# Performance work log

Hardware: AMD Instinct MI355X
Metric: run time of the kernel (lower is better)

The kernel has to match this reference:

```python
import jax, jax.numpy as jnp
import numpy as np

N = 16384      # total nodes (8 graphs x 2048)
E = 262144     # edges (avg degree 16)
TW = 25        # time_window
H = 128        # hidden_features
POS_DIM = 2
NB = 8         # number of graphs in batch
L = 6          # hidden_layer
DT = 0.01
EPS = 1e-5
MSG_IN = 2 * H + TW + POS_DIM + 1   # 284 (actual message concat width)
UPD_IN = H + H + 1                  # 257
EMB_IN = TW + POS_DIM + 1           # 28


def _lin(key, fan_in, fan_out):
    return jax.random.normal(key, (fan_in, fan_out), jnp.float32) / np.sqrt(fan_in)


def setup_inputs() -> dict:
    key = jax.random.key(0)
    ks = jax.random.split(key, 24)
    inp = {}
    inp["u"] = jax.random.normal(ks[0], (N, TW), jnp.float32)
    inp["pos"] = jax.random.uniform(ks[1], (N, 1 + POS_DIM), jnp.float32)
    inp["edge_index"] = jax.random.randint(ks[2], (2, E), 0, N)
    inp["batch"] = jnp.sort(jax.random.randint(ks[3], (N,), 0, NB))
    # embedding MLP
    inp["emb_W1"] = _lin(ks[4], EMB_IN, H); inp["emb_b1"] = jnp.zeros((H,), jnp.float32)
    inp["emb_W2"] = _lin(ks[5], H, H);      inp["emb_b2"] = jnp.zeros((H,), jnp.float32)
    # 6 GNN layers (stacked)
    inp["msg_W1"] = jax.vmap(lambda k: _lin(k, MSG_IN, H))(jax.random.split(ks[6], L))
    inp["msg_b1"] = jnp.zeros((L, H), jnp.float32)
    inp["msg_W2"] = jax.vmap(lambda k: _lin(k, H, H))(jax.random.split(ks[7], L))
    inp["msg_b2"] = jnp.zeros((L, H), jnp.float32)
    inp["upd_W1"] = jax.vmap(lambda k: _lin(k, UPD_IN, H))(jax.random.split(ks[8], L))
    inp["upd_b1"] = jnp.zeros((L, H), jnp.float32)
    inp["upd_W2"] = jax.vmap(lambda k: _lin(k, H, H))(jax.random.split(ks[9], L))
    inp["upd_b2"] = jnp.zeros((L, H), jnp.float32)
    # output CNN: Conv1d(1,8,15,s4) -> Conv1d(8,4,10,s2) -> Conv1d(4,1,10,s1)
    inp["conv1_W"] = jax.random.normal(ks[10], (8, 1, 15), jnp.float32) / np.sqrt(15)
    inp["conv1_b"] = jnp.zeros((8,), jnp.float32)
    inp["conv2_W"] = jax.random.normal(ks[11], (4, 8, 10), jnp.float32) / np.sqrt(80)
    inp["conv2_b"] = jnp.zeros((4,), jnp.float32)
    inp["conv3_W"] = jax.random.normal(ks[12], (1, 4, 10), jnp.float32) / np.sqrt(40)
    inp["conv3_b"] = jnp.zeros((1,), jnp.float32)
    return inp


def _mlp2(x, W1, b1, W2, b2):
    return jax.nn.relu(jax.nn.relu(x @ W1 + b1) @ W2 + b2)


def _instance_norm(h, batch):
    # PyG InstanceNorm (affine=False): per-graph, per-channel normalization
    cnt = jax.ops.segment_sum(jnp.ones((h.shape[0], 1), h.dtype), batch, NB)
    cnt = jnp.maximum(cnt, 1.0)
    mean = jax.ops.segment_sum(h, batch, NB) / cnt
    meansq = jax.ops.segment_sum(h * h, batch, NB) / cnt
    var = jnp.maximum(meansq - mean * mean, 0.0)
    return (h - mean[batch]) * jax.lax.rsqrt(var[batch] + EPS)


def _gnn_layer(h, u, pos_sp, variables, src, dst, batch,
               mW1, mb1, mW2, mb2, uW1, ub1, uW2, ub2):
    # message: gather endpoints, concat, 2-layer ReLU MLP  [E, MSG_IN] -> [E, H]
    m_in = jnp.concatenate([h[dst], h[src], u[dst] - u[src],
                            pos_sp[dst] - pos_sp[src], variables[dst]], axis=-1)
    msg = _mlp2(m_in, mW1, mb1, mW2, mb2)
    # mean-scatter aggregation onto target nodes
    deg = jax.ops.segment_sum(jnp.ones((src.shape[0], 1), h.dtype), dst, N)
    agg = jax.ops.segment_sum(msg, dst, N) / jnp.maximum(deg, 1.0)
    # node update MLP + residual (in_features == out_features)
    upd = _mlp2(jnp.concatenate([h, agg, variables], axis=-1), uW1, ub1, uW2, ub2)
    return _instance_norm(h + upd, batch)


def _conv1d(x, W, b, stride):
    # x: [N, C_in, L], W: [C_out, C_in, K]
    y = jax.lax.conv_general_dilated(x, W, (stride,), 'VALID',
                                     dimension_numbers=('NCH', 'OIH', 'NCH'))
    return y + b[None, :, None]


def reference(u, pos, edge_index, batch,
              emb_W1, emb_b1, emb_W2, emb_b2,
              msg_W1, msg_b1, msg_W2, msg_b2,
              upd_W1, upd_b1, upd_W2, upd_b2,
              conv1_W, conv1_b, conv2_W, conv2_b, conv3_W, conv3_b):
    variables = pos[:, 0:1]          # time variable
    pos_sp = pos[:, 1:1 + POS_DIM]   # spatial coords
    node_input = jnp.concatenate([u, pos_sp[:, 0:1], pos_sp[:, 1:2], variables], axis=-1)
    h = _mlp2(node_input, emb_W1, emb_b1, emb_W2, emb_b2)  # [N, H]
    src, dst = edge_index[0], edge_index[1]  # PyG: row 0 = source (j), row 1 = target (i)
    for l in range(L):
        h = _gnn_layer(h, u, pos_sp, variables, src, dst, batch,
                       msg_W1[l], msg_b1[l], msg_W2[l], msg_b2[l],
                       upd_W1[l], upd_b1[l], upd_W2[l], upd_b2[l])
    # output CNN: [N,1,128] -> [N,1,1]
    y = jax.nn.relu(_conv1d(h[:, None, :], conv1_W, conv1_b, 4))
    y = jax.nn.relu(_conv1d(y, conv2_W, conv2_b, 2))
    diff = _conv1d(y, conv3_W, conv3_b, 1)[:, 0, :]        # [N, 1]
    dt = jnp.cumsum(jnp.full((1, TW), DT, jnp.float32), axis=1)
    return u[:, -1:] + dt * diff                            # [N, TW]
```

## Files before the change

kernel.cpp:

```cpp
#include <hip/hip_runtime.h>

#define NN 16384
#define NE 262144
#define TWC 25
#define HC 128
#define NBC 8
#define LC 6
#define MINC 284
#define UINC 257
#define EINC 28
#define EPSC 1e-5
#define DTC 0.01f
#define SP 65

#define FMA32F(ACCF, A0, A1, A2, A3, W0, W1_)                  \
  do {                                                         \
    float wv[8] = {W0.x, W0.y, W0.z, W0.w,                     \
                   W1_.x, W1_.y, W1_.z, W1_.w};                \
    float av[4] = {A0, A1, A2, A3};                            \
    _Pragma("unroll") for (int i_ = 0; i_ < 4; ++i_)           \
      _Pragma("unroll") for (int j_ = 0; j_ < 8; ++j_)         \
        ACCF[i_][j_] = fmaf(av[i_], wv[j_], ACCF[i_][j_]);     \
  } while (0)

#define FLUSH32(ACCD, ACCF)                                    \
  do {                                                         \
    _Pragma("unroll") for (int i_ = 0; i_ < 4; ++i_)           \
      _Pragma("unroll") for (int j_ = 0; j_ < 8; ++j_) {       \
        ACCD[i_][j_] += (double)ACCF[i_][j_];                  \
        ACCF[i_][j_] = 0.f;                                    \
      }                                                        \
  } while (0)

#define KSTEP(ACCF, WV, ROW, KW)                               \
  do {                                                         \
    float a0_ = sm[(ROW) * SP + e0 + 0];                       \
    float a1_ = sm[(ROW) * SP + e0 + 1];                       \
    float a2_ = sm[(ROW) * SP + e0 + 2];                       \
    float a3_ = sm[(ROW) * SP + e0 + 3];                       \
    float4 w0_ = WV[(KW) * 32 + jg * 2];                       \
    float4 w1_ = WV[(KW) * 32 + jg * 2 + 1];                   \
    FMA32F(ACCF, a0_, a1_, a2_, a3_, w0_, w1_);                \
  } while (0)

#define KSTEPN(ACCF, WV, ROW, KW)                              \
  do {                                                         \
    float a0_ = sm[(ROW) * SP + e0 + 0];                       \
    float a1_ = sm[(ROW) * SP + e0 + 1];                       \
    float a2_ = sm[(ROW) * SP + e0 + 2];                       \
    float a3_ = sm[(ROW) * SP + e0 + 3];                       \
    float4 w0_ = WV[(KW) * 32 + jg * 2];                       \
    float4 w1_ = WV[(KW) * 32 + jg * 2 + 1];                   \
    FMA32F(ACCF, -a0_, -a1_, -a2_, -a3_, w0_, w1_);            \
  } while (0)


__global__ __launch_bounds__(256) void k_cnt(const int* __restrict__ dst,
                                             int* __restrict__ cnt) {
  int e = blockIdx.x * 256 + threadIdx.x;
  if (e < NE) atomicAdd(&cnt[dst[e]], 1);
}

__global__ __launch_bounds__(256) void k_scan(const int* __restrict__ cnt,
                                              int* __restrict__ rowptr,
                                              int* __restrict__ fill) {
  __shared__ int part[256];
  int t = threadIdx.x;
  int s = 0;
  for (int i = 0; i < 64; ++i) s += cnt[t * 64 + i];
  part[t] = s;
  __syncthreads();
  if (t == 0) {
    int r = 0;
    for (int i = 0; i < 256; ++i) { int v = part[i]; part[i] = r; r += v; }
  }
  __syncthreads();
  int r = part[t];
  for (int i = 0; i < 64; ++i) {
    int n = t * 64 + i;
    rowptr[n] = r;
    fill[n] = r;
    r += cnt[n];
  }
  if (t == 255) rowptr[NN] = r;
}

__global__ __launch_bounds__(256) void k_scatter(const int* __restrict__ src,
                                                 const int* __restrict__ dst,
                                                 int* __restrict__ fill,
                                                 int* __restrict__ srcS,
                                                 int* __restrict__ dstS) {
  int e = blockIdx.x * 256 + threadIdx.x;
  if (e < NE) {
    int d = dst[e];
    int p = atomicAdd(&fill[d], 1);
    srcS[p] = src[e];
    dstS[p] = d;
  }
}

__global__ __launch_bounds__(256) void k_rdeg(const int* __restrict__ rowptr,
                                              float* __restrict__ rdeg) {
  int n = blockIdx.x * 256 + threadIdx.x;
  if (n < NN) {
    int c = rowptr[n + 1] - rowptr[n];
    rdeg[n] = 1.0f / (float)max(c, 1);
  }
}

__global__ __launch_bounds__(256) void k_cntb(const int* __restrict__ batch,
                                              float* __restrict__ cntb) {
  int n = blockIdx.x * 256 + threadIdx.x;
  int b = (n < NN) ? batch[n] : -1;
#pragma unroll
  for (int bb = 0; bb < NBC; ++bb) {
    unsigned long long m = __ballot(b == bb);
    if ((threadIdx.x & 63) == 0 && m != 0ULL)
      atomicAdd(&cntb[bb], (float)__popcll(m));
  }
}

__global__ __launch_bounds__(256) void k_emb(
    const float* __restrict__ u, const float* __restrict__ pos,
    const float* __restrict__ W1, const float* __restrict__ b1,
    const float* __restrict__ W2, const float* __restrict__ b2,
    float* __restrict__ h) {
  __shared__ float sin_[2][EINC];
  __shared__ float shid[2][HC];
  int n0 = blockIdx.x * 2;
  int t = threadIdx.x;
  if (t < 2 * EINC) {
    int e = t / EINC, c = t - e * EINC;
    int n = n0 + e;
    float v;
    if (c < TWC) v = u[n * TWC + c];
    else if (c == TWC) v = pos[n * 3 + 1];
    else if (c == TWC + 1) v = pos[n * 3 + 2];
    else v = pos[n * 3 + 0];
    sin_[e][c] = v;
  }
  __syncthreads();
  int e = t >> 7, j = t & 127;
  double acc = (double)b1[j];
  for (int k = 0; k < EINC; ++k)
    acc = fma((double)sin_[e][k], (double)W1[k * HC + j], acc);
  shid[e][j] = fmaxf((float)acc, 0.f);
  __syncthreads();
  double acc2 = (double)b2[j];
  for (int k = 0; k < HC; ++k)
    acc2 = fma((double)shid[e][k], (double)W2[k * HC + j], acc2);
  h[(n0 + e) * HC + j] = fmaxf((float)acc2, 0.f);
}

__global__ __launch_bounds__(256) void k_node(
    const float* __restrict__ h, const float* __restrict__ u,
    const float* __restrict__ pos, const float* __restrict__ W1,
    const float* __restrict__ b1, float* __restrict__ Dv,
    float* __restrict__ Sv) {
  __shared__ float sm[156 * SP];
  const int t = threadIdx.x;
  const int n_base = blockIdx.x * 64;
  const int isS = blockIdx.y;
  const int eg = t >> 4, jg = t & 15;
  const int e0 = eg * 4, j0 = jg * 8;
  const int half = t >> 7, col = t & 127;

  for (int it = 0; it < 32; ++it) {
    int e = 2 * it + half;
    sm[col * SP + e] = h[(n_base + e) * HC + col];
  }
  for (int idx = t; idx < 64 * 28; idx += 256) {
    int e = idx / 28, c = idx - e * 28;
    int n = n_base + e;
    float v;
    if (c < TWC) v = u[n * TWC + c];
    else if (c == TWC) v = pos[n * 3 + 1];
    else if (c == TWC + 1) v = pos[n * 3 + 2];
    else v = pos[n * 3 + 0];
    sm[(128 + c) * SP + e] = v;
  }
  __syncthreads();

  float accf[4][8];
  double accd[4][8];
#pragma unroll
  for (int jj = 0; jj < 8; ++jj) {
    double bv = isS ? 0.0 : (double)b1[j0 + jj];
#pragma unroll
    for (int i = 0; i < 4; ++i) { accd[i][jj] = bv; accf[i][jj] = 0.f; }
  }

  const float4* W1v = (const float4*)W1;
  const int wb = isS ? 128 : 0;
  for (int kc = 0; kc < 128; kc += 32) {
#pragma unroll
    for (int kk = 0; kk < 32; ++kk) KSTEP(accf, W1v, kc + kk, wb + kc + kk);
    FLUSH32(accd, accf);
  }
  if (!isS) {
#pragma unroll
    for (int kk = 0; kk < 28; ++kk) KSTEP(accf, W1v, 128 + kk, 256 + kk);
  } else {
#pragma unroll
    for (int kk = 0; kk < 27; ++kk) KSTEPN(accf, W1v, 128 + kk, 256 + kk);
  }
  FLUSH32(accd, accf);

  float* outp = isS ? Sv : Dv;
#pragma unroll
  for (int i = 0; i < 4; ++i) {
    int n = n_base + e0 + i;
#pragma unroll
    for (int jj = 0; jj < 8; ++jj)
      outp[n * HC + j0 + jj] = (float)accd[i][jj];
  }
}

__global__ __launch_bounds__(256) void k_msg(
    const float* __restrict__ Dv, const float* __restrict__ Sv,
    const int* __restrict__ srcS, const int* __restrict__ dstS,
    const float* __restrict__ W2, const float* __restrict__ b2,
    float* __restrict__ agg) {
  __shared__ float sm[128 * SP];
  const int t = threadIdx.x;
  const int e_base = blockIdx.x * 64;
  const int eg = t >> 4, jg = t & 15;
  const int e0 = eg * 4, j0 = jg * 8;
  const int half = t >> 7, col = t & 127;

  if (t < 64) {
    sm[t * SP + 64] = __int_as_float(dstS[e_base + t]);
    sm[(64 + t) * SP + 64] = __int_as_float(srcS[e_base + t]);
  }
  __syncthreads();

  for (int it = 0; it < 32; ++it) {
    int e = 2 * it + half;
    int nd = __float_as_int(sm[e * SP + 64]);
    int ns = __float_as_int(sm[(64 + e) * SP + 64]);
    sm[col * SP + e] = fmaxf(Dv[nd * HC + col] + Sv[ns * HC + col], 0.f);
  }
  __syncthreads();

  float accf[4][8];
  double accd[4][8];
#pragma unroll
  for (int jj = 0; jj < 8; ++jj) {
    double bv = (double)b2[j0 + jj];
#pragma unroll
    for (int i = 0; i < 4; ++i) { accd[i][jj] = bv; accf[i][jj] = 0.f; }
  }

  const float4* W2v = (const float4*)W2;
  for (int kc = 0; kc < 128; kc += 32) {
#pragma unroll
    for (int kk = 0; kk < 32; ++kk) KSTEP(accf, W2v, kc + kk, kc + kk);
    FLUSH32(accd, accf);
  }
  __syncthreads();

#pragma unroll
  for (int jj = 0; jj < 8; ++jj) {
#pragma unroll
    for (int i = 0; i < 4; ++i)
      sm[(j0 + jj) * SP + e0 + i] = fmaxf((float)accd[i][jj], 0.f);
  }
  __syncthreads();

  {
    int j = t & 127;
    int ebeg = (t >> 7) * 32;
    float s = 0.f;
    int cur = __float_as_int(sm[ebeg * SP + 64]);
    for (int e = ebeg; e < ebeg + 32; ++e) {
      int d = __float_as_int(sm[e * SP + 64]);
      if (d != cur) {
        atomicAdd(&agg[cur * HC + j], s);
        s = 0.f;
        cur = d;
      }
      s += sm[j * SP + e];
    }
    atomicAdd(&agg[cur * HC + j], s);
  }
}

__global__ __launch_bounds__(256) void k_upd(
    const float* __restrict__ h, const float* __restrict__ pos,
    const float* __restrict__ agg, const float* __restrict__ rdeg,
    const float* __restrict__ W1, const float* __restrict__ b1,
    const float* __restrict__ W2, const float* __restrict__ b2,
    float* __restrict__ hn) {
  __shared__ float sm[129 * SP];
  const int t = threadIdx.x;
  const int n_base = blockIdx.x * 64;
  const int eg = t >> 4, jg = t & 15;
  const int e0 = eg * 4, j0 = jg * 8;
  const int half = t >> 7, col = t & 127;

  float accf[4][8];
  double accd[4][8];
#pragma unroll
  for (int jj = 0; jj < 8; ++jj) {
    double bv = (double)b1[j0 + jj];
#pragma unroll
    for (int i = 0; i < 4; ++i) { accd[i][jj] = bv; accf[i][jj] = 0.f; }
  }

  for (int it = 0; it < 32; ++it) {
    int e = 2 * it + half;
    sm[col * SP + e] = h[(n_base + e) * HC + col];
  }
  __syncthreads();

  const float4* W1v = (const float4*)W1;
  for (int kc = 0; kc < 128; kc += 32) {
#pragma unroll
    for (int kk = 0; kk < 32; ++kk) KSTEP(accf, W1v, kc + kk, kc + kk);
    FLUSH32(accd, accf);
  }
  __syncthreads();

  for (int it = 0; it < 32; ++it) {
    int e = 2 * it + half;
    int n = n_base + e;
    sm[col * SP + e] = agg[n * HC + col] * rdeg[n];
  }
  if (t < 64) sm[128 * SP + t] = pos[(n_base + t) * 3 + 0];
  __syncthreads();

  for (int kc = 0; kc < 128; kc += 32) {
#pragma unroll
    for (int kk = 0; kk < 32; ++kk) KSTEP(accf, W1v, kc + kk, 128 + kc + kk);
    FLUSH32(accd, accf);
  }
  KSTEP(accf, W1v, 128, 256);
  FLUSH32(accd, accf);
  __syncthreads();

#pragma unroll
  for (int jj = 0; jj < 8; ++jj) {
#pragma unroll
    for (int i = 0; i < 4; ++i)
      sm[(j0 + jj) * SP + e0 + i] = fmaxf((float)accd[i][jj], 0.f);
  }
  __syncthreads();

#pragma unroll
  for (int jj = 0; jj < 8; ++jj) {
    double bv = (double)b2[j0 + jj];
#pragma unroll
    for (int i = 0; i < 4; ++i) { accd[i][jj] = bv; accf[i][jj] = 0.f; }
  }
  const float4* W2v = (const float4*)W2;
  for (int kc = 0; kc < 128; kc += 32) {
#pragma unroll
    for (int kk = 0; kk < 32; ++kk) KSTEP(accf, W2v, kc + kk, kc + kk);
    FLUSH32(accd, accf);
  }

#pragma unroll
  for (int i = 0; i < 4; ++i) {
    int n = n_base + e0 + i;
#pragma unroll
    for (int jj = 0; jj < 8; ++jj) {
      int j = j0 + jj;
      hn[n * HC + j] = h[n * HC + j] + fmaxf((float)accd[i][jj], 0.f);
    }
  }
}

__global__ __launch_bounds__(256) void k_stats(const float* __restrict__ hn,
                                               const int* __restrict__ batch,
                                               double* __restrict__ stats) {
  int n0 = blockIdx.x * 32;
  int ch = threadIdx.x & 127;
  int rh = threadIdx.x >> 7;
  double s = 0.0, ss = 0.0;
  int cur = batch[n0 + rh];
  for (int r = rh; r < 32; r += 2) {
    int n = n0 + r;
    int b = batch[n];
    double v = (double)hn[n * HC + ch];
    if (b != cur) {
      atomicAdd(&stats[cur * HC + ch], s);
      atomicAdd(&stats[NBC * HC + cur * HC + ch], ss);
      s = 0.0; ss = 0.0; cur = b;
    }
    s += v;
    ss += v * v;
  }
  atomicAdd(&stats[cur * HC + ch], s);
  atomicAdd(&stats[NBC * HC + cur * HC + ch], ss);
}

__global__ __launch_bounds__(256) void k_norm(
    const float* __restrict__ hn, const int* __restrict__ batch,
    const double* __restrict__ stats, const float* __restrict__ cntb,
    float* __restrict__ hout) {
  int idx = blockIdx.x * 256 + threadIdx.x;
  int n = idx >> 7, ch = idx & 127;
  int b = batch[n];
  double c = fmax((double)cntb[b], 1.0);
  double mean = stats[b * HC + ch] / c;
  double ms = stats[NBC * HC + b * HC + ch] / c;
  double var = fmax(ms - mean * mean, 0.0);
  hout[idx] = (float)(((double)hn[idx] - mean) / sqrt(var + EPSC));
}

__global__ __launch_bounds__(64) void k_head(
    const float* __restrict__ h, const float* __restrict__ u,
    const float* __restrict__ c1W, const float* __restrict__ c1b,
    const float* __restrict__ c2W, const float* __restrict__ c2b,
    const float* __restrict__ c3W, const float* __restrict__ c3b,
    float* __restrict__ out) {
  __shared__ float hr[128];
  __shared__ float y1[8 * 29];
  __shared__ float y2[4 * 10];
  __shared__ float dv;
  int n = blockIdx.x, t = threadIdx.x;
  hr[t] = h[n * HC + t];
  hr[t + 64] = h[n * HC + 64 + t];
  __syncthreads();
  for (int idx = t; idx < 8 * 29; idx += 64) {
    int o = idx / 29, p = idx - o * 29;
    float acc = c1b[o];
    for (int q = 0; q < 15; ++q) acc = fmaf(hr[p * 4 + q], c1W[o * 15 + q], acc);
    y1[o * 29 + p] = fmaxf(acc, 0.f);
  }
  __syncthreads();
  if (t < 40) {
    int o = t / 10, p = t - o * 10;
    float acc = c2b[o];
    for (int i = 0; i < 8; ++i)
      for (int q = 0; q < 10; ++q)
        acc = fmaf(y1[i * 29 + p * 2 + q], c2W[o * 80 + i * 10 + q], acc);
    y2[o * 10 + p] = fmaxf(acc, 0.f);
  }
  __syncthreads();
  if (t == 0) {
    float acc = c3b[0];
    for (int i = 0; i < 4; ++i)
      for (int q = 0; q < 10; ++q)
        acc = fmaf(y2[i * 10 + q], c3W[i * 10 + q], acc);
    dv = acc;
  }
  __syncthreads();
  if (t < TWC) out[n * TWC + t] = u[n * TWC + 24] + DTC * (float)(t + 1) * dv;
}

extern "C" void kernel_launch(void* const* d_in, const int* in_sizes, int n_in,
                              void* d_out, int out_size, void* d_ws,
                              size_t ws_size, hipStream_t stream) {
  const float* u = (const float*)d_in[0];
  const float* pos = (const float*)d_in[1];
  const int* ei = (const int*)d_in[2];
  const int* batch = (const int*)d_in[3];
  const float* eW1 = (const float*)d_in[4];
  const float* eb1 = (const float*)d_in[5];
  const float* eW2 = (const float*)d_in[6];
  const float* eb2 = (const float*)d_in[7];
  const float* mW1 = (const float*)d_in[8];
  const float* mb1 = (const float*)d_in[9];
  const float* mW2 = (const float*)d_in[10];
  const float* mb2 = (const float*)d_in[11];
  const float* uW1 = (const float*)d_in[12];
  const float* ub1 = (const float*)d_in[13];
  const float* uW2 = (const float*)d_in[14];
  const float* ub2 = (const float*)d_in[15];
  const float* c1W = (const float*)d_in[16];
  const float* c1b = (const float*)d_in[17];
  const float* c2W = (const float*)d_in[18];
  const float* c2b = (const float*)d_in[19];
  const float* c3W = (const float*)d_in[20];
  const float* c3b = (const float*)d_in[21];
  float* out = (float*)d_out;

  const int* srcI = ei;
  const int* dstI = ei + NE;

  double* statsd = (double*)d_ws;
  float* h = (float*)(statsd + 2 * NBC * HC);
  float* Sv = h + NN * HC;
  float* agg = Sv + NN * HC;
  float* Dhn = agg + NN * HC;
  float* rdeg = Dhn + NN * HC;
  float* cntb = rdeg + NN;
  int* cnt = (int*)(cntb + NBC);
  int* rowptr = cnt + NN;
  int* fill = rowptr + NN + 1;
  int* srcS = fill + NN;
  int* dstS = srcS + NE;

  hipMemsetAsync(cnt, 0, NN * sizeof(int), stream);
  hipMemsetAsync(cntb, 0, NBC * sizeof(float), stream);
  k_cnt<<<NE / 256, 256, 0, stream>>>(dstI, cnt);
  k_scan<<<1, 256, 0, stream>>>(cnt, rowptr, fill);
  k_scatter<<<NE / 256, 256, 0, stream>>>(srcI, dstI, fill, srcS, dstS);
  k_rdeg<<<NN / 256, 256, 0, stream>>>(rowptr, rdeg);
  k_cntb<<<NN / 256, 256, 0, stream>>>(batch, cntb);
  k_emb<<<NN / 2, 256, 0, stream>>>(u, pos, eW1, eb1, eW2, eb2, h);

  for (int l = 0; l < LC; ++l) {
    hipMemsetAsync(agg, 0, (size_t)NN * HC * sizeof(float), stream);
    hipMemsetAsync(statsd, 0, 2 * NBC * HC * sizeof(double), stream);
    k_node<<<dim3(NN / 64, 2), 256, 0, stream>>>(
        h, u, pos, mW1 + (size_t)l * MINC * HC, mb1 + l * HC, Dhn, Sv);
    k_msg<<<NE / 64, 256, 0, stream>>>(Dhn, Sv, srcS, dstS,
                                       mW2 + (size_t)l * HC * HC, mb2 + l * HC,
                                       agg);
    k_upd<<<NN / 64, 256, 0, stream>>>(h, pos, agg, rdeg,
                                       uW1 + (size_t)l * UINC * HC, ub1 + l * HC,
                                       uW2 + (size_t)l * HC * HC, ub2 + l * HC,
                                       Dhn);
    k_stats<<<NN / 32, 256, 0, stream>>>(Dhn, batch, statsd);
    k_norm<<<NN * HC / 256, 256, 0, stream>>>(Dhn, batch, statsd, cntb, h);
  }
  k_head<<<NN, 64, 0, stream>>>(h, u, c1W, c1b, c2W, c2b, c3W, c3b, out);
}
```

Baseline: 2.140 ms.

## Fuse instance-norm stats into update kernel, merge node D/S passes, remap threads

Per-graph sum and sum-of-squares accumulation moves into the k_upd epilogue, so the separate k_stats kernel and its re-read of hn go away. k_node now computes both the destination and source projections in one block instead of launching a second grid dimension, which reuses the shared-memory staging of h but halves the grid and serialises the work. The thread-to-(row,col) mapping is swapped in node, msg and upd kernels, which changes the global store and weight-load access patterns. The fused stats issue more double atomics per thread (8 channels x 4 rows per thread instead of a 32-row reduction), which may add contention.

```diff
diff --git a/kernel.cpp b/kernel.cpp
--- a/kernel.cpp
+++ b/kernel.cpp
@@ -160,8 +160,7 @@
   __shared__ float sm[156 * SP];
   const int t = threadIdx.x;
   const int n_base = blockIdx.x * 64;
-  const int isS = blockIdx.y;
-  const int eg = t >> 4, jg = t & 15;
+  const int eg = t & 15, jg = t >> 4;
   const int e0 = eg * 4, j0 = jg * 8;
   const int half = t >> 7, col = t & 127;
 
@@ -181,38 +180,50 @@
   }
   __syncthreads();
 
+  const float4* W1v = (const float4*)W1;
   float accf[4][8];
   double accd[4][8];
-#pragma unroll
-  for (int jj = 0; jj < 8; ++jj) {
-    double bv = isS ? 0.0 : (double)b1[j0 + jj];
+
+#pragma unroll
+  for (int jj = 0; jj < 8; ++jj) {
+    double bv = (double)b1[j0 + jj];
 #pragma unroll
     for (int i = 0; i < 4; ++i) { accd[i][jj] = bv; accf[i][jj] = 0.f; }
   }
-
-  const float4* W1v = (const float4*)W1;
-  const int wb = isS ? 128 : 0;
   for (int kc = 0; kc < 128; kc += 32) {
 #pragma unroll
-    for (int kk = 0; kk < 32; ++kk) KSTEP(accf, W1v, kc + kk, wb + kc + kk);
+    for (int kk = 0; kk < 32; ++kk) KSTEP(accf, W1v, kc + kk, kc + kk);
     FLUSH32(accd, accf);
   }
-  if (!isS) {
-#pragma unroll
-    for (int kk = 0; kk < 28; ++kk) KSTEP(accf, W1v, 128 + kk, 256 + kk);
-  } else {
-#pragma unroll
-    for (int kk = 0; kk < 27; ++kk) KSTEPN(accf, W1v, 128 + kk, 256 + kk);
-  }
+#pragma unroll
+  for (int kk = 0; kk < 28; ++kk) KSTEP(accf, W1v, 128 + kk, 256 + kk);
   FLUSH32(accd, accf);
-
-  float* outp = isS ? Sv : Dv;
 #pragma unroll
   for (int i = 0; i < 4; ++i) {
     int n = n_base + e0 + i;
 #pragma unroll
     for (int jj = 0; jj < 8; ++jj)
-      outp[n * HC + j0 + jj] = (float)accd[i][jj];
+      Dv[n * HC + j0 + jj] = (float)accd[i][jj];
+  }
+
+#pragma unroll
+  for (int jj = 0; jj < 8; ++jj)
+#pragma unroll
+    for (int i = 0; i < 4; ++i) { accd[i][jj] = 0.0; accf[i][jj] = 0.f; }
+  for (int kc = 0; kc < 128; kc += 32) {
+#pragma unroll
+    for (int kk = 0; kk < 32; ++kk) KSTEP(accf, W1v, kc + kk, 128 + kc + kk);
+    FLUSH32(accd, accf);
+  }
+#pragma unroll
+  for (int kk = 0; kk < 27; ++kk) KSTEPN(accf, W1v, 128 + kk, 256 + kk);
+  FLUSH32(accd, accf);
+#pragma unroll
+  for (int i = 0; i < 4; ++i) {
+    int n = n_base + e0 + i;
+#pragma unroll
+    for (int jj = 0; jj < 8; ++jj)
+      Sv[n * HC + j0 + jj] = (float)accd[i][jj];
   }
 }
 
@@ -224,7 +235,7 @@
   __shared__ float sm[128 * SP];
   const int t = threadIdx.x;
   const int e_base = blockIdx.x * 64;
-  const int eg = t >> 4, jg = t & 15;
+  const int eg = t & 15, jg = t >> 4;
   const int e0 = eg * 4, j0 = jg * 8;
   const int half = t >> 7, col = t & 127;
 
@@ -288,13 +299,14 @@
 __global__ __launch_bounds__(256) void k_upd(
     const float* __restrict__ h, const float* __restrict__ pos,
     const float* __restrict__ agg, const float* __restrict__ rdeg,
-    const float* __restrict__ W1, const float* __restrict__ b1,
-    const float* __restrict__ W2, const float* __restrict__ b2,
-    float* __restrict__ hn) {
+    const int* __restrict__ batch, const float* __restrict__ W1,
+    const float* __restrict__ b1, const float* __restrict__ W2,
+    const float* __restrict__ b2, float* __restrict__ hn,
+    double* __restrict__ stats) {
   __shared__ float sm[129 * SP];
   const int t = threadIdx.x;
   const int n_base = blockIdx.x * 64;
-  const int eg = t >> 4, jg = t & 15;
+  const int eg = t & 15, jg = t >> 4;
   const int e0 = eg * 4, j0 = jg * 8;
   const int half = t >> 7, col = t & 127;
 
@@ -359,39 +371,37 @@
     FLUSH32(accd, accf);
   }
 
+  double s[8], ss[8];
+  int curb = batch[n_base + e0];
+#pragma unroll
+  for (int jj = 0; jj < 8; ++jj) { s[jj] = 0.0; ss[jj] = 0.0; }
 #pragma unroll
   for (int i = 0; i < 4; ++i) {
     int n = n_base + e0 + i;
+    int b = batch[n];
+    if (b != curb) {
+#pragma unroll
+      for (int jj = 0; jj < 8; ++jj) {
+        atomicAdd(&stats[curb * HC + j0 + jj], s[jj]);
+        atomicAdd(&stats[NBC * HC + curb * HC + j0 + jj], ss[jj]);
+        s[jj] = 0.0; ss[jj] = 0.0;
+      }
+      curb = b;
+    }
 #pragma unroll
     for (int jj = 0; jj < 8; ++jj) {
       int j = j0 + jj;
-      hn[n * HC + j] = h[n * HC + j] + fmaxf((float)accd[i][jj], 0.f);
+      float v = h[n * HC + j] + fmaxf((float)accd[i][jj], 0.f);
+      hn[n * HC + j] = v;
+      s[jj] += (double)v;
+      ss[jj] += (double)v * (double)v;
     }
   }
-}
-
-__global__ __launch_bounds__(256) void k_stats(const float* __restrict__ hn,
-                                               const int* __restrict__ batch,
-                                               double* __restrict__ stats) {
-  int n0 = blockIdx.x * 32;
-  int ch = threadIdx.x & 127;
-  int rh = threadIdx.x >> 7;
-  double s = 0.0, ss = 0.0;
-  int cur = batch[n0 + rh];
-  for (int r = rh; r < 32; r += 2) {
-    int n = n0 + r;
-    int b = batch[n];
-    double v = (double)hn[n * HC + ch];
-    if (b != cur) {
-      atomicAdd(&stats[cur * HC + ch], s);
-      atomicAdd(&stats[NBC * HC + cur * HC + ch], ss);
-      s = 0.0; ss = 0.0; cur = b;
-    }
-    s += v;
-    ss += v * v;
-  }
-  atomicAdd(&stats[cur * HC + ch], s);
-  atomicAdd(&stats[NBC * HC + cur * HC + ch], ss);
+#pragma unroll
+  for (int jj = 0; jj < 8; ++jj) {
+    atomicAdd(&stats[curb * HC + j0 + jj], s[jj]);
+    atomicAdd(&stats[NBC * HC + curb * HC + j0 + jj], ss[jj]);
+  }
 }
 
 __global__ __launch_bounds__(256) void k_norm(
@@ -504,16 +514,15 @@
   for (int l = 0; l < LC; ++l) {
     hipMemsetAsync(agg, 0, (size_t)NN * HC * sizeof(float), stream);
     hipMemsetAsync(statsd, 0, 2 * NBC * HC * sizeof(double), stream);
-    k_node<<<dim3(NN / 64, 2), 256, 0, stream>>>(
+    k_node<<<NN / 64, 256, 0, stream>>>(
         h, u, pos, mW1 + (size_t)l * MINC * HC, mb1 + l * HC, Dhn, Sv);
     k_msg<<<NE / 64, 256, 0, stream>>>(Dhn, Sv, srcS, dstS,
                                        mW2 + (size_t)l * HC * HC, mb2 + l * HC,
                                        agg);
-    k_upd<<<NN / 64, 256, 0, stream>>>(h, pos, agg, rdeg,
+    k_upd<<<NN / 64, 256, 0, stream>>>(h, pos, agg, rdeg, batch,
                                        uW1 + (size_t)l * UINC * HC, ub1 + l * HC,
                                        uW2 + (size_t)l * HC * HC, ub2 + l * HC,
-                                       Dhn);
-    k_stats<<<NN / 32, 256, 0, stream>>>(Dhn, batch, statsd);
+                                       Dhn, statsd);
     k_norm<<<NN * HC / 256, 256, 0, stream>>>(Dhn, batch, statsd, cntb, h);
   }
   k_head<<<NN, 64, 0, stream>>>(h, u, c1W, c1b, c2W, c2b, c3W, c3b, out);
```

Result: slower. 2.746 ms (+28.3%).

## Fold instance norm into consumers, pack FMAs in msg, swizzle msg block order

Applied to the files above, without the earlier changes.

Removes the standalone normalization pass by computing per-graph mean and inverse std in a tiny finalize kernel and applying normalization on the fly when k_node, k_upd and k_head load the hidden state. k_upd now updates the unnormalized buffer in place. The message kernel switches to packed two-wide float FMAs and remaps block indices so consecutive blocks are spread across edge ranges. These cut one full read and write of the hidden buffer per layer and aim to raise FMA throughput, but they add repeated double-precision normalization arithmetic inside the consumer kernels.

```diff
diff --git a/kernel.cpp b/kernel.cpp
--- a/kernel.cpp
+++ b/kernel.cpp
@@ -13,6 +13,8 @@
 #define DTC 0.01f
 #define SP 65
 
+typedef float v2f __attribute__((ext_vector_type(2)));
+
 #define FMA32F(ACCF, A0, A1, A2, A3, W0, W1_)                  \
   do {                                                         \
     float wv[8] = {W0.x, W0.y, W0.z, W0.w,                     \
@@ -52,6 +54,41 @@
     float4 w0_ = WV[(KW) * 32 + jg * 2];                       \
     float4 w1_ = WV[(KW) * 32 + jg * 2 + 1];                   \
     FMA32F(ACCF, -a0_, -a1_, -a2_, -a3_, w0_, w1_);            \
+  } while (0)
+
+#define KSTEPP(ACCF, WV, ROW, KW)                                        \
+  do {                                                                   \
+    v2f a01_ = {sm[(ROW) * SP + e0 + 0], sm[(ROW) * SP + e0 + 1]};       \
+    v2f a23_ = {sm[(ROW) * SP + e0 + 2], sm[(ROW) * SP + e0 + 3]};       \
+    float4 w0_ = WV[(KW) * 32 + jg * 2];                                 \
+    float4 w1_ = WV[(KW) * 32 + jg * 2 + 1];                             \
+    float wv_[8] = {w0_.x, w0_.y, w0_.z, w0_.w,                          \
+                    w1_.x, w1_.y, w1_.z, w1_.w};                         \
+    _Pragma("unroll") for (int j_ = 0; j_ < 8; ++j_) {                   \
+      v2f ws_ = {wv_[j_], wv_[j_]};                                      \
+      ACCF[0][j_] = __builtin_elementwise_fma(a01_, ws_, ACCF[0][j_]);   \
+      ACCF[1][j_] = __builtin_elementwise_fma(a23_, ws_, ACCF[1][j_]);   \
+    }                                                                    \
+  } while (0)
+
+#define FLUSH32P(ACCD, ACCF)                                             \
+  do {                                                                   \
+    _Pragma("unroll") for (int i_ = 0; i_ < 4; ++i_)                     \
+      _Pragma("unroll") for (int j_ = 0; j_ < 8; ++j_)                   \
+        ACCD[i_][j_] += (double)ACCF[i_ >> 1][j_][i_ & 1];               \
+    _Pragma("unroll") for (int i_ = 0; i_ < 2; ++i_)                     \
+      _Pragma("unroll") for (int j_ = 0; j_ < 8; ++j_)                   \
+        ACCF[i_][j_] = (v2f){0.f, 0.f};                                  \
+  } while (0)
+
+#define ACC_INIT(ACCD, ACCF, BV)                                         \
+  do {                                                                   \
+    _Pragma("unroll") for (int j_ = 0; j_ < 8; ++j_) {                   \
+      double bv_ = (BV);                                                 \
+      _Pragma("unroll") for (int i_ = 0; i_ < 4; ++i_) ACCD[i_][j_] = bv_; \
+      ACCF[0][j_] = (v2f){0.f, 0.f};                                     \
+      ACCF[1][j_] = (v2f){0.f, 0.f};                                     \
+    }                                                                    \
   } while (0)
 
 
@@ -120,11 +157,36 @@
   }
 }
 
+__global__ __launch_bounds__(256) void k_init(double* __restrict__ meanv,
+                                              double* __restrict__ invsd) {
+  int idx = blockIdx.x * 256 + threadIdx.x;
+  if (idx < NBC * HC) {
+    meanv[idx] = 0.0;
+    invsd[idx] = 1.0;
+  }
+}
+
+__global__ __launch_bounds__(256) void k_fin(const double* __restrict__ stats,
+                                             const float* __restrict__ cntb,
+                                             double* __restrict__ meanv,
+                                             double* __restrict__ invsd) {
+  int idx = blockIdx.x * 256 + threadIdx.x;
+  if (idx < NBC * HC) {
+    int b = idx >> 7;
+    double c = fmax((double)cntb[b], 1.0);
+    double mean = stats[idx] / c;
+    double ms = stats[NBC * HC + idx] / c;
+    double var = fmax(ms - mean * mean, 0.0);
+    meanv[idx] = mean;
+    invsd[idx] = 1.0 / sqrt(var + EPSC);
+  }
+}
+
 __global__ __launch_bounds__(256) void k_emb(
     const float* __restrict__ u, const float* __restrict__ pos,
     const float* __restrict__ W1, const float* __restrict__ b1,
     const float* __restrict__ W2, const float* __restrict__ b2,
-    float* __restrict__ h) {
+    float* __restrict__ hn) {
   __shared__ float sin_[2][EINC];
   __shared__ float shid[2][HC];
   int n0 = blockIdx.x * 2;
@@ -149,15 +211,17 @@
   double acc2 = (double)b2[j];
   for (int k = 0; k < HC; ++k)
     acc2 = fma((double)shid[e][k], (double)W2[k * HC + j], acc2);
-  h[(n0 + e) * HC + j] = fmaxf((float)acc2, 0.f);
+  hn[(n0 + e) * HC + j] = fmaxf((float)acc2, 0.f);
 }
 
 __global__ __launch_bounds__(256) void k_node(
-    const float* __restrict__ h, const float* __restrict__ u,
-    const float* __restrict__ pos, const float* __restrict__ W1,
-    const float* __restrict__ b1, float* __restrict__ Dv,
-    float* __restrict__ Sv) {
+    const float* __restrict__ hn, const double* __restrict__ meanv,
+    const double* __restrict__ invsd, const int* __restrict__ batch,
+    const float* __restrict__ u, const float* __restrict__ pos,
+    const float* __restrict__ W1, const float* __restrict__ b1,
+    float* __restrict__ Dv, float* __restrict__ Sv) {
   __shared__ float sm[156 * SP];
+  __shared__ int sbat[64];
   const int t = threadIdx.x;
   const int n_base = blockIdx.x * 64;
   const int isS = blockIdx.y;
@@ -165,9 +229,23 @@
   const int e0 = eg * 4, j0 = jg * 8;
   const int half = t >> 7, col = t & 127;
 
-  for (int it = 0; it < 32; ++it) {
-    int e = 2 * it + half;
-    sm[col * SP + e] = h[(n_base + e) * HC + col];
+  if (t < 64) sbat[t] = batch[n_base + t];
+  __syncthreads();
+
+  {
+    int curb = -1;
+    double mv = 0.0, iv = 1.0;
+    for (int it = 0; it < 32; ++it) {
+      int e = 2 * it + half;
+      int bn = sbat[e];
+      if (bn != curb) {
+        curb = bn;
+        mv = meanv[bn * HC + col];
+        iv = invsd[bn * HC + col];
+      }
+      sm[col * SP + e] =
+          (float)(((double)hn[(n_base + e) * HC + col] - mv) * iv);
+    }
   }
   for (int idx = t; idx < 64 * 28; idx += 256) {
     int e = idx / 28, c = idx - e * 28;
@@ -181,6 +259,7 @@
   }
   __syncthreads();
 
+  const float4* W1v = (const float4*)W1;
   float accf[4][8];
   double accd[4][8];
 #pragma unroll
@@ -190,7 +269,6 @@
     for (int i = 0; i < 4; ++i) { accd[i][jj] = bv; accf[i][jj] = 0.f; }
   }
 
-  const float4* W1v = (const float4*)W1;
   const int wb = isS ? 128 : 0;
   for (int kc = 0; kc < 128; kc += 32) {
 #pragma unroll
@@ -223,7 +301,8 @@
     float* __restrict__ agg) {
   __shared__ float sm[128 * SP];
   const int t = threadIdx.x;
-  const int e_base = blockIdx.x * 64;
+  const int bid = blockIdx.x;
+  const int e_base = ((bid & 7) * 512 + (bid >> 3)) * 64;
   const int eg = t >> 4, jg = t & 15;
   const int e0 = eg * 4, j0 = jg * 8;
   const int half = t >> 7, col = t & 127;
@@ -242,20 +321,15 @@
   }
   __syncthreads();
 
-  float accf[4][8];
+  v2f accf[2][8];
   double accd[4][8];
-#pragma unroll
-  for (int jj = 0; jj < 8; ++jj) {
-    double bv = (double)b2[j0 + jj];
-#pragma unroll
-    for (int i = 0; i < 4; ++i) { accd[i][jj] = bv; accf[i][jj] = 0.f; }
-  }
+  ACC_INIT(accd, accf, (double)b2[j0 + j_]);
 
   const float4* W2v = (const float4*)W2;
   for (int kc = 0; kc < 128; kc += 32) {
 #pragma unroll
-    for (int kk = 0; kk < 32; ++kk) KSTEP(accf, W2v, kc + kk, kc + kk);
-    FLUSH32(accd, accf);
+    for (int kk = 0; kk < 32; ++kk) KSTEPP(accf, W2v, kc + kk, kc + kk);
+    FLUSH32P(accd, accf);
   }
   __syncthreads();
 
@@ -286,18 +360,23 @@
 }
 
 __global__ __launch_bounds__(256) void k_upd(
-    const float* __restrict__ h, const float* __restrict__ pos,
-    const float* __restrict__ agg, const float* __restrict__ rdeg,
-    const float* __restrict__ W1, const float* __restrict__ b1,
-    const float* __restrict__ W2, const float* __restrict__ b2,
-    float* __restrict__ hn) {
+    float* __restrict__ hn, const double* __restrict__ meanv,
+    const double* __restrict__ invsd, const int* __restrict__ batch,
+    const float* __restrict__ pos, const float* __restrict__ agg,
+    const float* __restrict__ rdeg, const float* __restrict__ W1,
+    const float* __restrict__ b1, const float* __restrict__ W2,
+    const float* __restrict__ b2) {
   __shared__ float sm[129 * SP];
+  __shared__ int sbat[64];
   const int t = threadIdx.x;
   const int n_base = blockIdx.x * 64;
   const int eg = t >> 4, jg = t & 15;
   const int e0 = eg * 4, j0 = jg * 8;
   const int half = t >> 7, col = t & 127;
 
+  if (t < 64) sbat[t] = batch[n_base + t];
+  __syncthreads();
+
   float accf[4][8];
   double accd[4][8];
 #pragma unroll
@@ -307,9 +386,20 @@
     for (int i = 0; i < 4; ++i) { accd[i][jj] = bv; accf[i][jj] = 0.f; }
   }
 
-  for (int it = 0; it < 32; ++it) {
-    int e = 2 * it + half;
-    sm[col * SP + e] = h[(n_base + e) * HC + col];
+  {
+    int curb = -1;
+    double mv = 0.0, iv = 1.0;
+    for (int it = 0; it < 32; ++it) {
+      int e = 2 * it + half;
+      int bn = sbat[e];
+      if (bn != curb) {
+        curb = bn;
+        mv = meanv[bn * HC + col];
+        iv = invsd[bn * HC + col];
+      }
+      sm[col * SP + e] =
+          (float)(((double)hn[(n_base + e) * HC + col] - mv) * iv);
+    }
   }
   __syncthreads();
 
@@ -362,10 +452,14 @@
 #pragma unroll
   for (int i = 0; i < 4; ++i) {
     int n = n_base + e0 + i;
+    int bn = sbat[e0 + i];
 #pragma unroll
     for (int jj = 0; jj < 8; ++jj) {
       int j = j0 + jj;
-      hn[n * HC + j] = h[n * HC + j] + fmaxf((float)accd[i][jj], 0.f);
+      double mv = meanv[bn * HC + j];
+      double iv = invsd[bn * HC + j];
+      float base = (float)(((double)hn[n * HC + j] - mv) * iv);
+      hn[n * HC + j] = base + fmaxf((float)accd[i][jj], 0.f);
     }
   }
 }
@@ -394,33 +488,23 @@
   atomicAdd(&stats[NBC * HC + cur * HC + ch], ss);
 }
 
-__global__ __launch_bounds__(256) void k_norm(
-    const float* __restrict__ hn, const int* __restrict__ batch,
-    const double* __restrict__ stats, const float* __restrict__ cntb,
-    float* __restrict__ hout) {
-  int idx = blockIdx.x * 256 + threadIdx.x;
-  int n = idx >> 7, ch = idx & 127;
-  int b = batch[n];
-  double c = fmax((double)cntb[b], 1.0);
-  double mean = stats[b * HC + ch] / c;
-  double ms = stats[NBC * HC + b * HC + ch] / c;
-  double var = fmax(ms - mean * mean, 0.0);
-  hout[idx] = (float)(((double)hn[idx] - mean) / sqrt(var + EPSC));
-}
-
 __global__ __launch_bounds__(64) void k_head(
-    const float* __restrict__ h, const float* __restrict__ u,
-    const float* __restrict__ c1W, const float* __restrict__ c1b,
-    const float* __restrict__ c2W, const float* __restrict__ c2b,
-    const float* __restrict__ c3W, const float* __restrict__ c3b,
-    float* __restrict__ out) {
+    const float* __restrict__ hn, const double* __restrict__ meanv,
+    const double* __restrict__ invsd, const int* __restrict__ batch,
+    const float* __restrict__ u, const float* __restrict__ c1W,
+    const float* __restrict__ c1b, const float* __restrict__ c2W,
+    const float* __restrict__ c2b, const float* __restrict__ c3W,
+    const float* __restrict__ c3b, float* __restrict__ out) {
   __shared__ float hr[128];
   __shared__ float y1[8 * 29];
   __shared__ float y2[4 * 10];
   __shared__ float dv;
   int n = blockIdx.x, t = threadIdx.x;
-  hr[t] = h[n * HC + t];
-  hr[t + 64] = h[n * HC + 64 + t];
+  int b = batch[n];
+  hr[t] = (float)(((double)hn[n * HC + t] - meanv[b * HC + t]) *
+                  invsd[b * HC + t]);
+  hr[t + 64] = (float)(((double)hn[n * HC + 64 + t] - meanv[b * HC + 64 + t]) *
+                       invsd[b * HC + 64 + t]);
   __syncthreads();
   for (int idx = t; idx < 8 * 29; idx += 64) {
     int o = idx / 29, p = idx - o * 29;
@@ -480,11 +564,13 @@
   const int* dstI = ei + NE;
 
   double* statsd = (double*)d_ws;
-  float* h = (float*)(statsd + 2 * NBC * HC);
-  float* Sv = h + NN * HC;
+  double* meanv = statsd + 2 * NBC * HC;
+  double* invsd = meanv + NBC * HC;
+  float* hn = (float*)(invsd + NBC * HC);
+  float* Sv = hn + NN * HC;
   float* agg = Sv + NN * HC;
-  float* Dhn = agg + NN * HC;
-  float* rdeg = Dhn + NN * HC;
+  float* Dv = agg + NN * HC;
+  float* rdeg = Dv + NN * HC;
   float* cntb = rdeg + NN;
   int* cnt = (int*)(cntb + NBC);
   int* rowptr = cnt + NN;
@@ -499,22 +585,24 @@
   k_scatter<<<NE / 256, 256, 0, stream>>>(srcI, dstI, fill, srcS, dstS);
   k_rdeg<<<NN / 256, 256, 0, stream>>>(rowptr, rdeg);
   k_cntb<<<NN / 256, 256, 0, stream>>>(batch, cntb);
-  k_emb<<<NN / 2, 256, 0, stream>>>(u, pos, eW1, eb1, eW2, eb2, h);
+  k_init<<<4, 256, 0, stream>>>(meanv, invsd);
+  k_emb<<<NN / 2, 256, 0, stream>>>(u, pos, eW1, eb1, eW2, eb2, hn);
 
   for (int l = 0; l < LC; ++l) {
     hipMemsetAsync(agg, 0, (size_t)NN * HC * sizeof(float), stream);
     hipMemsetAsync(statsd, 0, 2 * NBC * HC * sizeof(double), stream);
     k_node<<<dim3(NN / 64, 2), 256, 0, stream>>>(
-        h, u, pos, mW1 + (size_t)l * MINC * HC, mb1 + l * HC, Dhn, Sv);
-    k_msg<<<NE / 64, 256, 0, stream>>>(Dhn, Sv, srcS, dstS,
+        hn, meanv, invsd, batch, u, pos, mW1 + (size_t)l * MINC * HC,
+        mb1 + l * HC, Dv, Sv);
+    k_msg<<<NE / 64, 256, 0, stream>>>(Dv, Sv, srcS, dstS,
                                        mW2 + (size_t)l * HC * HC, mb2 + l * HC,
                                        agg);
-    k_upd<<<NN / 64, 256, 0, stream>>>(h, pos, agg, rdeg,
+    k_upd<<<NN / 64, 256, 0, stream>>>(hn, meanv, invsd, batch, pos, agg, rdeg,
                                        uW1 + (size_t)l * UINC * HC, ub1 + l * HC,
-                                       uW2 + (size_t)l * HC * HC, ub2 + l * HC,
-                                       Dhn);
-    k_stats<<<NN / 32, 256, 0, stream>>>(Dhn, batch, statsd);
-    k_norm<<<NN * HC / 256, 256, 0, stream>>>(Dhn, batch, statsd, cntb, h);
-  }
-  k_head<<<NN, 64, 0, stream>>>(h, u, c1W, c1b, c2W, c2b, c3W, c3b, out);
-}
+                                       uW2 + (size_t)l * HC * HC, ub2 + l * HC);
+    k_stats<<<NN / 32, 256, 0, stream>>>(hn, batch, statsd);
+    k_fin<<<4, 256, 0, stream>>>(statsd, cntb, meanv, invsd);
+  }
+  k_head<<<NN, 64, 0, stream>>>(hn, meanv, invsd, batch, u, c1W, c1b, c2W, c2b,
+                                c3W, c3b, out);
+}
```

Result: no change. 2.171 ms (+1.5%).
